# Performance work log

Measured on AMD Instinct MI355X. Metric: run time of the kernel, lower is better.

The kernel has to match this reference:

```python
import jax, jax.numpy as jnp
import numpy as np

EPS = 1e-8

def _l2norm(x):
    return x / (jnp.linalg.norm(x, axis=-1, keepdims=True) + EPS)

def setup_inputs() -> dict:
    key = jax.random.key(0)
    k1, k2, k3, k4, k5, k6 = jax.random.split(key, 6)
    NQ, NB, NF = 16384, 128, 64
    HD = 2 * NF
    Q = jax.random.normal(k1, (NQ, HD), dtype=jnp.float32)
    reference_angles = jax.random.uniform(k2, (NF,), dtype=jnp.float32) * 2.0 * np.pi
    probes = jax.random.normal(k3, (NB, HD), dtype=jnp.float32)
    # params: perturb around the torch inits (log(e-1), zeros, zeros) for a non-degenerate test
    init_val = float(np.log(np.e - 1.0))
    q_weights_raw = init_val + 0.1 * jax.random.normal(k4, (NB, NF), dtype=jnp.float32)
    q_magnitude_weights = 0.1 * jax.random.normal(k5, (NB, NF), dtype=jnp.float32)
    q_bias = 0.1 * jax.random.normal(k6, (NB,), dtype=jnp.float32)
    return {"Q": Q, "reference_angles": reference_angles, "probes": probes,
            "q_weights_raw": q_weights_raw, "q_magnitude_weights": q_magnitude_weights,
            "q_bias": q_bias}

def reference(Q, reference_angles, probes, q_weights_raw, q_magnitude_weights, q_bias):
    NF = reference_angles.shape[0]
    # --- shared probe layer: L2 normalize then RoPE-rotate (front/back real/imag layout)
    pn = _l2norm(probes)                      # (B, 2F)
    pr, pi = pn[:, :NF], pn[:, NF:]
    c, s = jnp.cos(reference_angles), jnp.sin(reference_angles)
    P_real = pr * c - pi * s                  # (B, F)
    P_imag = pr * s + pi * c
    # --- distance-based scorer
    Qn = _l2norm(Q)                           # (Nq, 2F)
    Q_real, Q_imag = Qn[:, :NF], Qn[:, NF:]
    err_r = P_real[None, :, :] - Q_real[:, None, :]   # (Nq, B, F)
    err_i = P_imag[None, :, :] - Q_imag[:, None, :]
    distance = jnp.sqrt(err_r ** 2 + err_i ** 2 + EPS)
    eff_w = -jax.nn.softplus(q_weights_raw)           # (B, F), negative weights
    distance_term = jnp.einsum('qbf,bf->qb', distance, eff_w)
    Q_mag = jnp.sqrt(Q_real ** 2 + Q_imag ** 2 + EPS)  # (Nq, F)
    magnitude_term = Q_mag @ q_magnitude_weights.T     # (Nq, B)
    return distance_term + magnitude_term + q_bias
```

## Files before the change

### kernel.cpp

```cpp
#include <hip/hip_runtime.h>

#define NQ 16384
#define NB 128
#define NF 64
#define HD 128
#define EPSF 1e-8f
#define BTILE 8
#define NBT (NB / BTILE)

struct FRow {
    float4 d[BTILE];
    float  m[BTILE];
};

__global__ __launch_bounds__(256) void prep_kernel(
    const float* __restrict__ Q,
    const float* __restrict__ probes,
    const float* __restrict__ angles,
    const float* __restrict__ qw,
    const float* __restrict__ mw,
    float4* __restrict__ qvals,
    FRow* __restrict__ tab) {
    if (blockIdx.x < 2048) {
        const int q  = blockIdx.x * 8 + (threadIdx.x >> 5);
        const int sl = threadIdx.x & 31;
        const float2* Q2 = (const float2*)Q;
        float2 a = Q2[q * 64 + sl];
        float2 c = Q2[q * 64 + 32 + sl];
        float ss = a.x * a.x + a.y * a.y + c.x * c.x + c.y * c.y;
        #pragma unroll
        for (int m = 1; m < 32; m <<= 1) ss += __shfl_xor(ss, m);
        float inv = 1.0f / (sqrtf(ss) + EPSF);
        float Qr0 = a.x * inv, Qr1 = a.y * inv;
        float Qi0 = c.x * inv, Qi1 = c.y * inv;
        float B0 = Qr0 * Qr0 + Qi0 * Qi0;
        float B1 = Qr1 * Qr1 + Qi1 * Qi1;
        qvals[(size_t)q * NF + 2 * sl]     = make_float4(Qr0, Qi0, B0, sqrtf(B0 + EPSF));
        qvals[(size_t)q * NF + 2 * sl + 1] = make_float4(Qr1, Qi1, B1, sqrtf(B1 + EPSF));
    } else {
        const int b    = (blockIdx.x - 2048) * 4 + (threadIdx.x >> 6);
        const int lane = threadIdx.x & 63;
        float p0 = probes[b * HD + lane];
        float p1 = probes[b * HD + 64 + lane];
        float ss = p0 * p0 + p1 * p1;
        #pragma unroll
        for (int m = 1; m < 64; m <<= 1) ss += __shfl_xor(ss, m);
        float inv = 1.0f / (sqrtf(ss) + EPSF);
        float pr = p0 * inv, pi = p1 * inv;
        float ang = angles[lane];
        float cc = cosf(ang), sn = sinf(ang);
        float Pr = pr * cc - pi * sn;
        float Pi = pr * sn + pi * cc;
        float x = qw[b * NF + lane];
        float sp = (x > 0.0f) ? (x + log1pf(expf(-x))) : log1pf(expf(x));
        FRow* r = &tab[(b >> 3) * NF + lane];
        r->d[b & 7] = make_float4(-2.0f * Pr, -2.0f * Pi, Pr * Pr + Pi * Pi + EPSF, -sp);
        r->m[b & 7] = mw[b * NF + lane];
    }
}

__global__ __launch_bounds__(256, 4) void main_kernel(
    const FRow* __restrict__ tab,
    const float4* __restrict__ qvals,
    const float* __restrict__ bias,
    float* __restrict__ out) {
    const int bt   = blockIdx.x & (NBT - 1);
    const int qblk = blockIdx.x / NBT;
    const int q = qblk * 256 + (threadIdx.x >> 6) * 64 + (threadIdx.x & 63);

    const FRow* __restrict__ tr = tab + bt * NF;
    const float4* __restrict__ qp = qvals + (size_t)q * NF;

    float acc[BTILE];
    #pragma unroll
    for (int i = 0; i < BTILE; ++i) acc[i] = 0.0f;

    #pragma unroll 4
    for (int f = 0; f < NF; ++f) {
        float4 qv = qp[f];
        #pragma unroll
        for (int bb = 0; bb < BTILE; ++bb) {
            float4 td = tr[f].d[bb];
            float tm  = tr[f].m[bb];
            float t = td.z + qv.z;
            t = fmaf(td.y, qv.y, t);
            t = fmaf(td.x, qv.x, t);
            t = fmaxf(t, 0.0f);
            float d = __builtin_amdgcn_sqrtf(t);
            acc[bb] = fmaf(td.w, d, acc[bb]);
            acc[bb] = fmaf(tm, qv.w, acc[bb]);
        }
    }

    #pragma unroll
    for (int bb = 0; bb < BTILE; ++bb) acc[bb] += bias[bt * BTILE + bb];
    float* op = out + (size_t)q * NB + bt * BTILE;
    *(float4*)op       = make_float4(acc[0], acc[1], acc[2], acc[3]);
    *(float4*)(op + 4) = make_float4(acc[4], acc[5], acc[6], acc[7]);
}

extern "C" void kernel_launch(void* const* d_in, const int* in_sizes, int n_in,
                              void* d_out, int out_size, void* d_ws, size_t ws_size,
                              hipStream_t stream) {
    const float* Q      = (const float*)d_in[0];
    const float* angles = (const float*)d_in[1];
    const float* probes = (const float*)d_in[2];
    const float* qw     = (const float*)d_in[3];
    const float* mw     = (const float*)d_in[4];
    const float* bias   = (const float*)d_in[5];
    float* out = (float*)d_out;

    char* ws = (char*)d_ws;
    FRow*   tab   = (FRow*)ws;
    float4* qvals = (float4*)(ws + NBT * NF * sizeof(FRow));

    prep_kernel<<<2048 + NB / 4, 256, 0, stream>>>(Q, probes, angles, qw, mw, qvals, tab);
    main_kernel<<<(NQ / 256) * NBT, 256, 0, stream>>>(tab, qvals, bias, out);
}
```

Baseline: 110.1 us.

## Stage probe table tile in LDS and halve probe tile per block

Changes the probe table layout to a plain feature-major array and has each block copy its tile into shared memory before the main loop, so the inner loop reads LDS instead of scalar/global loads. BTILE drops from 8 to 4, which doubles the grid. Each query's qvals row is now re-read 32 times instead of 16. The occupancy hint rises to 8 blocks, and fmax is replaced by fabs before sqrt. The trade-off is more redundant qvals traffic and output writes of 16 bytes instead of 32 per thread.

```diff
diff --git a/kernel.cpp b/kernel.cpp
--- a/kernel.cpp
+++ b/kernel.cpp
@@ -5,13 +5,14 @@
 #define NF 64
 #define HD 128
 #define EPSF 1e-8f
-#define BTILE 8
+#define BTILE 4
 #define NBT (NB / BTILE)
 
-struct FRow {
-    float4 d[BTILE];
-    float  m[BTILE];
-};
+__device__ __forceinline__ float wave_allreduce_sum(float v) {
+    #pragma unroll
+    for (int m = 1; m < 64; m <<= 1) v += __shfl_xor(v, m, 64);
+    return v;
+}
 
 __global__ __launch_bounds__(256) void prep_kernel(
     const float* __restrict__ Q,
@@ -20,7 +21,8 @@
     const float* __restrict__ qw,
     const float* __restrict__ mw,
     float4* __restrict__ qvals,
-    FRow* __restrict__ tab) {
+    float4* __restrict__ tableD,
+    float* __restrict__ tableM) {
     if (blockIdx.x < 2048) {
         const int q  = blockIdx.x * 8 + (threadIdx.x >> 5);
         const int sl = threadIdx.x & 31;
@@ -42,9 +44,7 @@
         const int lane = threadIdx.x & 63;
         float p0 = probes[b * HD + lane];
         float p1 = probes[b * HD + 64 + lane];
-        float ss = p0 * p0 + p1 * p1;
-        #pragma unroll
-        for (int m = 1; m < 64; m <<= 1) ss += __shfl_xor(ss, m);
+        float ss = wave_allreduce_sum(p0 * p0 + p1 * p1);
         float inv = 1.0f / (sqrtf(ss) + EPSF);
         float pr = p0 * inv, pi = p1 * inv;
         float ang = angles[lane];
@@ -53,50 +53,59 @@
         float Pi = pr * sn + pi * cc;
         float x = qw[b * NF + lane];
         float sp = (x > 0.0f) ? (x + log1pf(expf(-x))) : log1pf(expf(x));
-        FRow* r = &tab[(b >> 3) * NF + lane];
-        r->d[b & 7] = make_float4(-2.0f * Pr, -2.0f * Pi, Pr * Pr + Pi * Pi + EPSF, -sp);
-        r->m[b & 7] = mw[b * NF + lane];
+        tableD[lane * NB + b] = make_float4(-2.0f * Pr, -2.0f * Pi,
+                                            Pr * Pr + Pi * Pi + EPSF, -sp);
+        tableM[lane * NB + b] = mw[b * NF + lane];
     }
 }
 
-__global__ __launch_bounds__(256, 4) void main_kernel(
-    const FRow* __restrict__ tab,
+__global__ __launch_bounds__(256, 8) void main_kernel(
+    const float4* __restrict__ tableD,
+    const float* __restrict__ tableM,
     const float4* __restrict__ qvals,
     const float* __restrict__ bias,
     float* __restrict__ out) {
+    __shared__ __align__(16) float4 ldsD[NF * BTILE];
+    __shared__ __align__(16) float  ldsM[NF * BTILE];
     const int bt   = blockIdx.x & (NBT - 1);
     const int qblk = blockIdx.x / NBT;
-    const int q = qblk * 256 + (threadIdx.x >> 6) * 64 + (threadIdx.x & 63);
+    const int q = qblk * 256 + (int)threadIdx.x;
 
-    const FRow* __restrict__ tr = tab + bt * NF;
-    const float4* __restrict__ qp = qvals + (size_t)q * NF;
+    {
+        int idx = threadIdx.x;
+        int f = idx >> 2, bb = idx & 3;
+        ldsD[idx] = tableD[f * NB + bt * BTILE + bb];
+        ldsM[idx] = tableM[f * NB + bt * BTILE + bb];
+    }
+    __syncthreads();
 
     float acc[BTILE];
     #pragma unroll
     for (int i = 0; i < BTILE; ++i) acc[i] = 0.0f;
 
+    const float4* __restrict__ qp = qvals + (size_t)q * NF;
+
     #pragma unroll 4
     for (int f = 0; f < NF; ++f) {
         float4 qv = qp[f];
+        float4 tm4 = *(const float4*)&ldsM[f * BTILE];
         #pragma unroll
         for (int bb = 0; bb < BTILE; ++bb) {
-            float4 td = tr[f].d[bb];
-            float tm  = tr[f].m[bb];
+            float4 td = ldsD[f * BTILE + bb];
             float t = td.z + qv.z;
             t = fmaf(td.y, qv.y, t);
             t = fmaf(td.x, qv.x, t);
-            t = fmaxf(t, 0.0f);
-            float d = __builtin_amdgcn_sqrtf(t);
+            float d = __builtin_amdgcn_sqrtf(fabsf(t));
+            float w = (&tm4.x)[bb];
             acc[bb] = fmaf(td.w, d, acc[bb]);
-            acc[bb] = fmaf(tm, qv.w, acc[bb]);
+            acc[bb] = fmaf(w, qv.w, acc[bb]);
         }
     }
 
     #pragma unroll
     for (int bb = 0; bb < BTILE; ++bb) acc[bb] += bias[bt * BTILE + bb];
     float* op = out + (size_t)q * NB + bt * BTILE;
-    *(float4*)op       = make_float4(acc[0], acc[1], acc[2], acc[3]);
-    *(float4*)(op + 4) = make_float4(acc[4], acc[5], acc[6], acc[7]);
+    *(float4*)op = make_float4(acc[0], acc[1], acc[2], acc[3]);
 }
 
 extern "C" void kernel_launch(void* const* d_in, const int* in_sizes, int n_in,
@@ -111,9 +120,12 @@
     float* out = (float*)d_out;
 
     char* ws = (char*)d_ws;
-    FRow*   tab   = (FRow*)ws;
-    float4* qvals = (float4*)(ws + NBT * NF * sizeof(FRow));
+    float4* tableD = (float4*)ws;
+    float*  tableM = (float*)(ws + NF * NB * sizeof(float4));
+    float4* qvals  = (float4*)(ws + NF * NB * sizeof(float4)
+                                  + NF * NB * sizeof(float));
 
-    prep_kernel<<<2048 + NB / 4, 256, 0, stream>>>(Q, probes, angles, qw, mw, qvals, tab);
-    main_kernel<<<(NQ / 256) * NBT, 256, 0, stream>>>(tab, qvals, bias, out);
+    prep_kernel<<<2048 + NB / 4, 256, 0, stream>>>(Q, probes, angles, qw, mw,
+                                                   qvals, tableD, tableM);
+    main_kernel<<<(NQ / 256) * NBT, 256, 0, stream>>>(tableD, tableM, qvals, bias, out);
 }
```

After: 147.6 us. 1.34x slower.
